# Performance work log

Hardware: AMD Instinct MI355X
Metric: run time of the kernel (lower is better)

Reference implementation:

```python
import jax, jax.numpy as jnp
import numpy as np

EMBED = 64
TEMPERATURE = 8.0
LN_EPS = 1e-6


def setup_inputs() -> dict:
    key = jax.random.key(0)
    ks = jax.random.split(key, 9)
    n_map, n_obs = 16384, 8192
    s = 1.0 / np.sqrt(EMBED)
    return {
        "map_code": jax.random.normal(ks[0], (n_map, EMBED), jnp.float32),
        "obs_code": jax.random.normal(ks[1], (n_obs, EMBED), jnp.float32),
        "Wq": jax.random.normal(ks[2], (EMBED, EMBED), jnp.float32) * s,
        "Wk": jax.random.normal(ks[3], (EMBED, EMBED), jnp.float32) * s,
        "Wv": jax.random.normal(ks[4], (EMBED, EMBED), jnp.float32) * s,
        "Wo": jax.random.normal(ks[5], (EMBED // 2, EMBED), jnp.float32) * (1.0 / np.sqrt(EMBED // 2)),
        "bo": jnp.zeros((EMBED,), jnp.float32),
        "gamma": jnp.ones((EMBED,), jnp.float32),
        "beta": jnp.zeros((EMBED,), jnp.float32),
    }


def _glu(x):
    a, b = jnp.split(x, 2, axis=-1)
    return a * jax.nn.sigmoid(b)


def reference(map_code, obs_code, Wq, Wk, Wv, Wo, bo, gamma, beta):
    # projections (x @ W == torch Linear with weight W.T; params are random either way)
    map_q = map_code @ Wq          # [Nm, E]
    map_k = map_code @ Wk          # [Nm, E]
    map_v = map_code @ Wv          # [Nm, E]
    obs_k = obs_code @ Wk          # [No, E]
    obs_v = obs_code @ Wv          # [No, E]

    self_score = jnp.sum(map_q * map_k, axis=-1, keepdims=True)   # [Nm, 1]
    obs_score = map_q @ obs_k.T                                   # [Nm, No]
    w = jax.nn.softmax(
        jnp.concatenate([self_score, obs_score], axis=-1) / TEMPERATURE,
        axis=-1,
    )  # [Nm, 1+No]

    # GLU gating: glu(obs_v) is identical for every map row, so the original's
    # [Nm, 1+No, E] broadcast collapses to a rank-2 contraction.
    gated_map = _glu(map_v)   # [Nm, E/2]
    gated_obs = _glu(obs_v)   # [No, E/2]
    agg = w[:, :1] * gated_map + w[:, 1:] @ gated_obs   # [Nm, E/2]

    out = agg @ Wo + bo + map_code   # [Nm, E]
    mu = jnp.mean(out, axis=-1, keepdims=True)
    var = jnp.mean(jnp.square(out - mu), axis=-1, keepdims=True)
    return (out - mu) * jax.lax.rsqrt(var + LN_EPS) * gamma + beta
```

## Files before the change

### kernel.cpp

```cpp
#include <hip/hip_runtime.h>
#include <hip/hip_bf16.h>


typedef float f32x16 __attribute__((ext_vector_type(16)));
typedef short bf16x8 __attribute__((ext_vector_type(8)));
typedef unsigned int u32;

__device__ __forceinline__ u32 cvt_pk_bf16(float lo, float hi) {
    u32 r;
    asm("v_cvt_pk_bf16_f32 %0, %1, %2" : "=v"(r) : "v"(lo), "v"(hi));
    return r;
}
__device__ __forceinline__ void permswap32(u32& a, u32& b) {
    asm("v_permlane32_swap_b32 %0, %1" : "+v"(a), "+v"(b));
}

#define IT 0.18033688011112042f
#define LOG2E 1.44269504089f

__global__ __launch_bounds__(256) void prep_kernel(
    const float* __restrict__ map_code, const float* __restrict__ obs_code,
    const float* __restrict__ Wq, const float* __restrict__ Wk,
    const float* __restrict__ Wv,
    __hip_bfloat16* __restrict__ qbf, __hip_bfloat16* __restrict__ Kp,
    __hip_bfloat16* __restrict__ Vp, float* __restrict__ pself,
    float* __restrict__ gmT, int n_map, int n_obs)
{
    __shared__ float xs[32 * 64];
    const int t = threadIdx.x;
    const int w = t >> 6;
    const int e = t & 63;
    const int r0 = blockIdx.x * 32;
    const int total = n_map + n_obs;

    #pragma unroll
    for (int i = 0; i < 8; ++i) {
        const int idx = i * 256 + t;
        const int gr = r0 + (idx >> 6);
        const int col = idx & 63;
        float val = 0.0f;
        if (gr < n_map)      val = map_code[(size_t)gr * 64 + col];
        else if (gr < total) val = obs_code[(size_t)(gr - n_map) * 64 + col];
        xs[idx] = val;
    }
    __syncthreads();

    float qa[8] = {}, ka[8] = {}, va[8] = {};
    const float* xw = xs + (w * 8) * 64;
    #pragma unroll 4
    for (int d = 0; d < 64; ++d) {
        const float wq = Wq[d * 64 + e];
        const float wk = Wk[d * 64 + e];
        const float wv = Wv[d * 64 + e];
        #pragma unroll
        for (int i = 0; i < 8; ++i) {
            const float x = xw[i * 64 + d];
            qa[i] = fmaf(x, wq, qa[i]);
            ka[i] = fmaf(x, wk, ka[i]);
            va[i] = fmaf(x, wv, va[i]);
        }
    }

    #pragma unroll
    for (int i = 0; i < 8; ++i) {
        const int r = r0 + w * 8 + i;
        if (r >= total) break;
        const bool is_map = r < n_map;
        const float vother = __shfl_xor(va[i], 32);
        const float sig = 1.0f / (1.0f + __builtin_amdgcn_exp2f(-vother * LOG2E));
        const float g = va[i] * sig;

        if (is_map) {
            qbf[(size_t)r * 64 + e] = __float2bfloat16(qa[i] * IT);
            float qk = qa[i] * ka[i];
            #pragma unroll
            for (int off = 32; off; off >>= 1) qk += __shfl_xor(qk, off);
            if (e == 0) pself[r] = __builtin_amdgcn_exp2f(qk * IT);
            if (e < 32) gmT[(size_t)e * n_map + r] = g;
        } else {
            const int j  = r - n_map;
            const int kb = j >> 5, jq = j & 31;
            {
                const int c = e >> 4, h2 = (e >> 3) & 1, ii = e & 7;
                Kp[(size_t)kb * 2048 + c * 512 + (h2 * 32 + jq) * 8 + ii] =
                    __float2bfloat16(ka[i]);
            }
            if (e < 32) {
                const int h = jq >> 4, h3 = (jq >> 3) & 1, ii = jq & 7;
                Vp[(size_t)kb * 1024 + h * 512 + (h3 * 32 + e) * 8 + ii] =
                    __float2bfloat16(g);
            }
        }
    }
}

#define WAVES 8
__global__ __launch_bounds__(64 * WAVES, 4) void attn_partial(
    const __hip_bfloat16* __restrict__ qbf, const __hip_bfloat16* __restrict__ Kp,
    const __hip_bfloat16* __restrict__ Vp,
    __hip_bfloat16* __restrict__ oP, float* __restrict__ lP,
    int n_obs, int n_map, int kslog)
{
    const int tid  = threadIdx.x;
    const int w    = tid >> 6;
    const int lane = tid & 63;
    const int ql   = lane & 31;
    const int hi   = lane >> 5;
    const int qb   = blockIdx.x >> kslog;
    const int slice= blockIdx.x & ((1 << kslog) - 1);
    const int tileT= qb * WAVES + w;
    const int q    = tileT * 32 + ql;

    __shared__ __align__(16) char kl[32768 + 16384];
    char* vl = kl + 32768;

    bf16x8 qf[4];
    {
        const __hip_bfloat16* qrow = qbf + (size_t)q * 64 + 8 * hi;
        #pragma unroll
        for (int c = 0; c < 4; ++c)
            qf[c] = *reinterpret_cast<const bf16x8*>(qrow + c * 16);
    }

    float lsumA = 0.0f, lsumB = 0.0f;
    f32x16 o = {};

    const int nkb      = (n_obs >> kslog) >> 5;
    const int kb_begin = slice * nkb;
    const char* Kb = (const char*)Kp;
    const char* Vb = (const char*)Vp;

    auto body = [&](const bf16x8 (&kf)[4], const bf16x8 (&vf)[2]) {
        f32x16 s = {};
        #pragma unroll
        for (int c = 0; c < 4; ++c)
            s = __builtin_amdgcn_mfma_f32_32x32x16_bf16(kf[c], qf[c], s, 0, 0, 0);
        float p[16];
        #pragma unroll
        for (int r = 0; r < 16; ++r) p[r] = __builtin_amdgcn_exp2f(s[r]);
        #pragma unroll
        for (int r = 0; r < 8; ++r) { lsumA += p[r]; lsumB += p[r + 8]; }
        union { u32 u[4]; bf16x8 v; } pb0, pb1;
        {
            u32 x0 = cvt_pk_bf16(p[0], p[1]);
            u32 x1 = cvt_pk_bf16(p[2], p[3]);
            u32 y0 = cvt_pk_bf16(p[4], p[5]);
            u32 y1 = cvt_pk_bf16(p[6], p[7]);
            permswap32(x0, y0);
            permswap32(x1, y1);
            pb0.u[0] = x0; pb0.u[1] = x1; pb0.u[2] = y0; pb0.u[3] = y1;
        }
        {
            u32 x0 = cvt_pk_bf16(p[8],  p[9]);
            u32 x1 = cvt_pk_bf16(p[10], p[11]);
            u32 y0 = cvt_pk_bf16(p[12], p[13]);
            u32 y1 = cvt_pk_bf16(p[14], p[15]);
            permswap32(x0, y0);
            permswap32(x1, y1);
            pb1.u[0] = x0; pb1.u[1] = x1; pb1.u[2] = y0; pb1.u[3] = y1;
        }
        o = __builtin_amdgcn_mfma_f32_32x32x16_bf16(vf[0], pb0.v, o, 0, 0, 0);
        o = __builtin_amdgcn_mfma_f32_32x32x16_bf16(vf[1], pb1.v, o, 0, 0, 0);
    };

    for (int c0 = 0; c0 < nkb; c0 += 8) {
        if (c0) __syncthreads();
        const char* Ks = Kb + (size_t)(kb_begin + c0) * 4096;
        const char* Vs = Vb + (size_t)(kb_begin + c0) * 2048;
        #pragma unroll
        for (int i = 0; i < 4; ++i) {
            const int idx = i * 512 + tid;
            *reinterpret_cast<uint4*>(kl + idx * 16) =
                *reinterpret_cast<const uint4*>(Ks + idx * 16);
        }
        #pragma unroll
        for (int i = 0; i < 2; ++i) {
            const int idx = i * 512 + tid;
            *reinterpret_cast<uint4*>(vl + idx * 16) =
                *reinterpret_cast<const uint4*>(Vs + idx * 16);
        }
        __syncthreads();

        #pragma unroll 2
        for (int kb = 0; kb < 8; ++kb) {
            bf16x8 kf[4], vf[2];
            const char* kbp = kl + kb * 4096 + lane * 16;
            #pragma unroll
            for (int c = 0; c < 4; ++c)
                kf[c] = *reinterpret_cast<const bf16x8*>(kbp + c * 1024);
            const char* vbp = vl + kb * 2048 + lane * 16;
            vf[0] = *reinterpret_cast<const bf16x8*>(vbp);
            vf[1] = *reinterpret_cast<const bf16x8*>(vbp + 1024);
            body(kf, vf);
        }
    }

    float lsum = lsumA + lsumB;
    lsum += __shfl_xor(lsum, 32);
    if (hi == 0) lP[(size_t)slice * n_map + tileT * 32 + ql] = lsum;
    __hip_bfloat16* ob = oP + ((size_t)slice * (n_map >> 5) + tileT) * 1024;
    #pragma unroll
    for (int r = 0; r < 16; ++r) {
        const int vr = (r & 3) + 8 * (r >> 2) + 4 * hi;
        ob[vr * 32 + ql] = __float2bfloat16(o[r]);
    }
}

__global__ __launch_bounds__(256) void reduce_oP(
    const __hip_bfloat16* __restrict__ oP, const float* __restrict__ pself,
    const float* __restrict__ gmT, float* __restrict__ agg,
    int n_map, int ks)
{
    const int gid = blockIdx.x * 256 + threadIdx.x;
    const int e0  = gid * 8;
    const int T   = e0 >> 10;
    const int t0  = e0 & 1023;
    const int v   = t0 >> 5;
    const int qq0 = t0 & 31;
    const int q0  = T * 32 + qq0;
    const int ntiles = n_map >> 5;

    float a[8];
    {
        const float4 ps0 = *reinterpret_cast<const float4*>(pself + q0);
        const float4 ps1 = *reinterpret_cast<const float4*>(pself + q0 + 4);
        const float4 g0  = *reinterpret_cast<const float4*>(gmT + (size_t)v * n_map + q0);
        const float4 g1  = *reinterpret_cast<const float4*>(gmT + (size_t)v * n_map + q0 + 4);
        a[0] = ps0.x * g0.x; a[1] = ps0.y * g0.y;
        a[2] = ps0.z * g0.z; a[3] = ps0.w * g0.w;
        a[4] = ps1.x * g1.x; a[5] = ps1.y * g1.y;
        a[6] = ps1.z * g1.z; a[7] = ps1.w * g1.w;
    }
    const __hip_bfloat16* ob = oP + (size_t)T * 1024 + t0;
    const size_t sstride = (size_t)ntiles * 1024;
    #pragma unroll 4
    for (int s = 0; s < ks; ++s) {
        const uint4 u = *reinterpret_cast<const uint4*>(ob + s * sstride);
        a[0] += __uint_as_float(u.x << 16);
        a[1] += __uint_as_float(u.x & 0xffff0000u);
        a[2] += __uint_as_float(u.y << 16);
        a[3] += __uint_as_float(u.y & 0xffff0000u);
        a[4] += __uint_as_float(u.z << 16);
        a[5] += __uint_as_float(u.z & 0xffff0000u);
        a[6] += __uint_as_float(u.w << 16);
        a[7] += __uint_as_float(u.w & 0xffff0000u);
    }
    float4* dst = reinterpret_cast<float4*>(agg + e0);
    dst[0] = make_float4(a[0], a[1], a[2], a[3]);
    dst[1] = make_float4(a[4], a[5], a[6], a[7]);
}

__global__ __launch_bounds__(256) void epilogue(
    const float* __restrict__ agg, const float* __restrict__ lP,
    const float* __restrict__ pself, const float* __restrict__ map_code,
    const float* __restrict__ Wo, const float* __restrict__ bo,
    const float* __restrict__ gamma, const float* __restrict__ beta,
    float* __restrict__ out, int n_map, int ks)
{
    const int tid  = threadIdx.x;
    const int w    = tid >> 6;
    const int lane = tid & 63;
    const int T    = blockIdx.x;
    const int q0   = T * 32;

    __shared__ float aggT[32][33];
    __shared__ float lsumL[8][32];
    __shared__ float invS[32];

    {
        const int g  = tid >> 5;
        const int qq = tid & 31;
        float part = 0.0f;
        for (int s = g; s < ks; s += 8)
            part += lP[(size_t)s * n_map + q0 + qq];
        lsumL[g][qq] = part;
    }
    {
        const float4 f4 = reinterpret_cast<const float4*>(agg + (size_t)T * 1024)[tid];
        const int v  = tid >> 3;
        const int qq = (tid & 7) * 4;
        aggT[v][qq + 0] = f4.x; aggT[v][qq + 1] = f4.y;
        aggT[v][qq + 2] = f4.z; aggT[v][qq + 3] = f4.w;
    }
    __syncthreads();
    if (tid < 32) {
        float l = pself[q0 + tid];
        #pragma unroll
        for (int g = 0; g < 8; ++g) l += lsumL[g][tid];
        invS[tid] = 1.0f / l;
    }
    __syncthreads();

    float wo[32];
    #pragma unroll
    for (int vv = 0; vv < 32; ++vv) wo[vv] = Wo[vv * 64 + lane];
    const float bo_e = bo[lane], ga = gamma[lane], be = beta[lane];

    #pragma unroll
    for (int i = 0; i < 8; ++i) {
        const int qq = w * 8 + i;
        float dot = 0.0f;
        #pragma unroll
        for (int vv = 0; vv < 32; ++vv)
            dot = fmaf(aggT[vv][qq], wo[vv], dot);
        float acc = dot * invS[qq] + bo_e + map_code[(size_t)(q0 + qq) * 64 + lane];
        float mu = acc;
        #pragma unroll
        for (int off = 32; off; off >>= 1) mu += __shfl_xor(mu, off);
        mu *= (1.0f / 64.0f);
        const float dc = acc - mu;
        float var = dc * dc;
        #pragma unroll
        for (int off = 32; off; off >>= 1) var += __shfl_xor(var, off);
        var *= (1.0f / 64.0f);
        out[(size_t)(q0 + qq) * 64 + lane] =
            dc * rsqrtf(var + 1e-6f) * ga + be;
    }
}

extern "C" void kernel_launch(void* const* d_in, const int* in_sizes, int n_in,
                              void* d_out, int out_size, void* d_ws, size_t ws_size,
                              hipStream_t stream) {
    const float* map_code = (const float*)d_in[0];
    const float* obs_code = (const float*)d_in[1];
    const float* Wq  = (const float*)d_in[2];
    const float* Wk  = (const float*)d_in[3];
    const float* Wv  = (const float*)d_in[4];
    const float* Wo  = (const float*)d_in[5];
    const float* bo  = (const float*)d_in[6];
    const float* gam = (const float*)d_in[7];
    const float* bet = (const float*)d_in[8];
    const int n_map = in_sizes[0] / 64;
    const int n_obs = in_sizes[1] / 64;
    const int ntiles = n_map / 32;

    char* ws = (char*)d_ws;
    __hip_bfloat16* qbf = (__hip_bfloat16*)ws; ws += (size_t)n_map * 64 * 2;
    __hip_bfloat16* Kp  = (__hip_bfloat16*)ws; ws += (size_t)n_obs * 64 * 2;
    __hip_bfloat16* Vp  = (__hip_bfloat16*)ws; ws += (size_t)n_obs * 32 * 2;
    float* pself        = (float*)ws;          ws += (size_t)n_map * 4;
    float* gmT          = (float*)ws;          ws += (size_t)n_map * 32 * 4;
    float* agg          = (float*)ws;          ws += (size_t)ntiles * 1024 * 4;
    const size_t base   = (size_t)(ws - (char*)d_ws);
    const size_t per_slice = (size_t)n_map * 32 * 2 + (size_t)n_map * 4;
    int kslog = 5;
    while (kslog > 0 && base + ((size_t)1 << kslog) * per_slice > ws_size)
        --kslog;
    const int ks = 1 << kslog;
    __hip_bfloat16* oP = (__hip_bfloat16*)ws; ws += (size_t)ks * n_map * 32 * 2;
    float* lP = (float*)ws;

    const int total = n_map + n_obs;
    prep_kernel<<<(total + 31) / 32, 256, 0, stream>>>(
        map_code, obs_code, Wq, Wk, Wv, qbf, Kp, Vp, pself, gmT,
        n_map, n_obs);
    attn_partial<<<(n_map / 256) * ks, 64 * WAVES, 0, stream>>>(
        qbf, Kp, Vp, oP, lP, n_obs, n_map, kslog);
    reduce_oP<<<(ntiles * 1024) / (256 * 8), 256, 0, stream>>>(
        oP, pself, gmT, agg, n_map, ks);
    epilogue<<<ntiles, 256, 0, stream>>>(
        agg, lP, pself, map_code, Wo, bo, gam, bet,
        (float*)d_out, n_map, ks);
}
```

Before: 67.20 us.

## Fuse split-K reduction into epilogue and halve attention LDS staging chunk

```diff
diff --git a/kernel.cpp b/kernel.cpp
--- a/kernel.cpp
+++ b/kernel.cpp
@@ -95,7 +95,7 @@
 }
 
 #define WAVES 8
-__global__ __launch_bounds__(64 * WAVES, 4) void attn_partial(
+__global__ __launch_bounds__(64 * WAVES, 8) void attn_partial(
     const __hip_bfloat16* __restrict__ qbf, const __hip_bfloat16* __restrict__ Kp,
     const __hip_bfloat16* __restrict__ Vp,
     __hip_bfloat16* __restrict__ oP, float* __restrict__ lP,
@@ -111,8 +111,8 @@
     const int tileT= qb * WAVES + w;
     const int q    = tileT * 32 + ql;
 
-    __shared__ __align__(16) char kl[32768 + 16384];
-    char* vl = kl + 32768;
+    __shared__ __align__(16) char kl[16384 + 8192];
+    char* vl = kl + 16384;
 
     bf16x8 qf[4];
     {
@@ -163,26 +163,24 @@
         o = __builtin_amdgcn_mfma_f32_32x32x16_bf16(vf[1], pb1.v, o, 0, 0, 0);
     };
 
-    for (int c0 = 0; c0 < nkb; c0 += 8) {
+    for (int c0 = 0; c0 < nkb; c0 += 4) {
         if (c0) __syncthreads();
         const char* Ks = Kb + (size_t)(kb_begin + c0) * 4096;
         const char* Vs = Vb + (size_t)(kb_begin + c0) * 2048;
         #pragma unroll
-        for (int i = 0; i < 4; ++i) {
+        for (int i = 0; i < 2; ++i) {
             const int idx = i * 512 + tid;
             *reinterpret_cast<uint4*>(kl + idx * 16) =
                 *reinterpret_cast<const uint4*>(Ks + idx * 16);
         }
-        #pragma unroll
-        for (int i = 0; i < 2; ++i) {
-            const int idx = i * 512 + tid;
-            *reinterpret_cast<uint4*>(vl + idx * 16) =
-                *reinterpret_cast<const uint4*>(Vs + idx * 16);
+        {
+            *reinterpret_cast<uint4*>(vl + tid * 16) =
+                *reinterpret_cast<const uint4*>(Vs + tid * 16);
         }
         __syncthreads();
 
         #pragma unroll 2
-        for (int kb = 0; kb < 8; ++kb) {
+        for (int kb = 0; kb < 4; ++kb) {
             bf16x8 kf[4], vf[2];
             const char* kbp = kl + kb * 4096 + lane * 16;
             #pragma unroll
@@ -206,62 +204,20 @@
     }
 }
 
-__global__ __launch_bounds__(256) void reduce_oP(
-    const __hip_bfloat16* __restrict__ oP, const float* __restrict__ pself,
-    const float* __restrict__ gmT, float* __restrict__ agg,
+__global__ __launch_bounds__(256) void combine_epi(
+    const __hip_bfloat16* __restrict__ oP, const float* __restrict__ lP,
+    const float* __restrict__ pself, const float* __restrict__ gmT,
+    const float* __restrict__ map_code, const float* __restrict__ Wo,
+    const float* __restrict__ bo, const float* __restrict__ gamma,
+    const float* __restrict__ beta, float* __restrict__ out,
     int n_map, int ks)
-{
-    const int gid = blockIdx.x * 256 + threadIdx.x;
-    const int e0  = gid * 8;
-    const int T   = e0 >> 10;
-    const int t0  = e0 & 1023;
-    const int v   = t0 >> 5;
-    const int qq0 = t0 & 31;
-    const int q0  = T * 32 + qq0;
-    const int ntiles = n_map >> 5;
-
-    float a[8];
-    {
-        const float4 ps0 = *reinterpret_cast<const float4*>(pself + q0);
-        const float4 ps1 = *reinterpret_cast<const float4*>(pself + q0 + 4);
-        const float4 g0  = *reinterpret_cast<const float4*>(gmT + (size_t)v * n_map + q0);
-        const float4 g1  = *reinterpret_cast<const float4*>(gmT + (size_t)v * n_map + q0 + 4);
-        a[0] = ps0.x * g0.x; a[1] = ps0.y * g0.y;
-        a[2] = ps0.z * g0.z; a[3] = ps0.w * g0.w;
-        a[4] = ps1.x * g1.x; a[5] = ps1.y * g1.y;
-        a[6] = ps1.z * g1.z; a[7] = ps1.w * g1.w;
-    }
-    const __hip_bfloat16* ob = oP + (size_t)T * 1024 + t0;
-    const size_t sstride = (size_t)ntiles * 1024;
-    #pragma unroll 4
-    for (int s = 0; s < ks; ++s) {
-        const uint4 u = *reinterpret_cast<const uint4*>(ob + s * sstride);
-        a[0] += __uint_as_float(u.x << 16);
-        a[1] += __uint_as_float(u.x & 0xffff0000u);
-        a[2] += __uint_as_float(u.y << 16);
-        a[3] += __uint_as_float(u.y & 0xffff0000u);
-        a[4] += __uint_as_float(u.z << 16);
-        a[5] += __uint_as_float(u.z & 0xffff0000u);
-        a[6] += __uint_as_float(u.w << 16);
-        a[7] += __uint_as_float(u.w & 0xffff0000u);
-    }
-    float4* dst = reinterpret_cast<float4*>(agg + e0);
-    dst[0] = make_float4(a[0], a[1], a[2], a[3]);
-    dst[1] = make_float4(a[4], a[5], a[6], a[7]);
-}
-
-__global__ __launch_bounds__(256) void epilogue(
-    const float* __restrict__ agg, const float* __restrict__ lP,
-    const float* __restrict__ pself, const float* __restrict__ map_code,
-    const float* __restrict__ Wo, const float* __restrict__ bo,
-    const float* __restrict__ gamma, const float* __restrict__ beta,
-    float* __restrict__ out, int n_map, int ks)
 {
     const int tid  = threadIdx.x;
     const int w    = tid >> 6;
     const int lane = tid & 63;
     const int T    = blockIdx.x;
     const int q0   = T * 32;
+    const int ntiles = n_map >> 5;
 
     __shared__ float aggT[32][33];
     __shared__ float lsumL[8][32];
@@ -275,12 +231,31 @@
             part += lP[(size_t)s * n_map + q0 + qq];
         lsumL[g][qq] = part;
     }
+
     {
-        const float4 f4 = reinterpret_cast<const float4*>(agg + (size_t)T * 1024)[tid];
-        const int v  = tid >> 3;
-        const int qq = (tid & 7) * 4;
-        aggT[v][qq + 0] = f4.x; aggT[v][qq + 1] = f4.y;
-        aggT[v][qq + 2] = f4.z; aggT[v][qq + 3] = f4.w;
+        const int e0  = tid * 4;
+        const int v   = e0 >> 5;
+        const int qq0 = e0 & 31;
+        float a[4];
+        {
+            const float4 ps = *reinterpret_cast<const float4*>(pself + q0 + qq0);
+            const float4 g4 = *reinterpret_cast<const float4*>(
+                gmT + (size_t)v * n_map + q0 + qq0);
+            a[0] = ps.x * g4.x; a[1] = ps.y * g4.y;
+            a[2] = ps.z * g4.z; a[3] = ps.w * g4.w;
+        }
+        const __hip_bfloat16* ob = oP + (size_t)T * 1024 + e0;
+        const size_t sstride = (size_t)ntiles * 1024;
+        #pragma unroll 4
+        for (int s = 0; s < ks; ++s) {
+            const uint2 u = *reinterpret_cast<const uint2*>(ob + s * sstride);
+            a[0] += __uint_as_float(u.x << 16);
+            a[1] += __uint_as_float(u.x & 0xffff0000u);
+            a[2] += __uint_as_float(u.y << 16);
+            a[3] += __uint_as_float(u.y & 0xffff0000u);
+        }
+        aggT[v][qq0 + 0] = a[0]; aggT[v][qq0 + 1] = a[1];
+        aggT[v][qq0 + 2] = a[2]; aggT[v][qq0 + 3] = a[3];
     }
     __syncthreads();
     if (tid < 32) {
@@ -340,7 +315,6 @@
     __hip_bfloat16* Vp  = (__hip_bfloat16*)ws; ws += (size_t)n_obs * 32 * 2;
     float* pself        = (float*)ws;          ws += (size_t)n_map * 4;
     float* gmT          = (float*)ws;          ws += (size_t)n_map * 32 * 4;
-    float* agg          = (float*)ws;          ws += (size_t)ntiles * 1024 * 4;
     const size_t base   = (size_t)(ws - (char*)d_ws);
     const size_t per_slice = (size_t)n_map * 32 * 2 + (size_t)n_map * 4;
     int kslog = 5;
@@ -356,9 +330,7 @@
         n_map, n_obs);
     attn_partial<<<(n_map / 256) * ks, 64 * WAVES, 0, stream>>>(
         qbf, Kp, Vp, oP, lP, n_obs, n_map, kslog);
-    reduce_oP<<<(ntiles * 1024) / (256 * 8), 256, 0, stream>>>(
-        oP, pself, gmT, agg, n_map, ks);
-    epilogue<<<ntiles, 256, 0, stream>>>(
-        agg, lP, pself, map_code, Wo, bo, gam, bet,
+    combine_epi<<<ntiles, 256, 0, stream>>>(
+        oP, lP, pself, gmT, map_code, Wo, bo, gam, bet,
         (float*)d_out, n_map, ks);
 }
```

Measured after the change: 153.7 us. 129% more time.
